# Kernel optimization log

Hardware: AMD Instinct MI355X
Metric: run time of the kernel (lower is better)

The kernel has to match this reference:

```python
import jax, jax.numpy as jnp
import numpy as np

NUM_MEMORIES = 4096
FEATURES = 4096
NUM_HEADS = 16
THRESHOLD = 1.0 / NUM_MEMORIES
EPSILON = 1e-12
COS_EPS = 1e-8
ENTROPY_COEF = 0.0002


def setup_inputs() -> dict:
    key = jax.random.key(0)
    ks = jax.random.split(key, 10)
    B, C, H, W = 256, 256, 4, 4
    F = FEATURES
    bound = float(np.sqrt(6.0 / F))  # kaiming_uniform fan_in = features
    x = jax.random.normal(ks[0], (B, C, H, W), dtype=jnp.float32)
    memory = jax.random.uniform(ks[1], (NUM_MEMORIES, F), minval=-bound, maxval=bound, dtype=jnp.float32)
    s = 0.02
    Wq = jax.random.normal(ks[2], (F, F), dtype=jnp.float32) * s
    Wk = jax.random.normal(ks[3], (F, F), dtype=jnp.float32) * s
    Wv = jax.random.normal(ks[4], (F, F), dtype=jnp.float32) * s
    Wo = jax.random.normal(ks[5], (F, F), dtype=jnp.float32) * s
    bq = jax.random.normal(ks[6], (F,), dtype=jnp.float32) * s
    bk = jax.random.normal(ks[7], (F,), dtype=jnp.float32) * s
    bv = jax.random.normal(ks[8], (F,), dtype=jnp.float32) * s
    bo = jax.random.normal(ks[9], (F,), dtype=jnp.float32) * s
    return {"x": x, "memory": memory, "Wq": Wq, "bq": bq, "Wk": Wk, "bk": bk,
            "Wv": Wv, "bv": bv, "Wo": Wo, "bo": bo}


def _mha(z, Wq, bq, Wk, bk, Wv, bv, Wo, bo):
    # z: [B, C, F] with C == 1 (seq_len = 1 here)
    B, C, F = z.shape
    dk = F // NUM_HEADS
    q = (z @ Wq + bq).reshape(B, C, NUM_HEADS, dk).transpose(0, 2, 1, 3)
    k = (z @ Wk + bk).reshape(B, C, NUM_HEADS, dk).transpose(0, 2, 1, 3)
    v = (z @ Wv + bv).reshape(B, C, NUM_HEADS, dk).transpose(0, 2, 1, 3)
    scores = jnp.einsum('bhqd,bhkd->bhqk', q, k) / jnp.sqrt(jnp.float32(dk))
    w = jax.nn.softmax(scores, axis=-1)
    o = jnp.einsum('bhqk,bhkd->bhqd', w, v).transpose(0, 2, 1, 3).reshape(B, C, F)
    return o @ Wo + bo


def reference(x, memory, Wq, bq, Wk, bk, Wv, bv, Wo, bo):
    B = x.shape[0]
    z = x.reshape(B, -1)[:, None, :]                      # [B, 1, F]
    z = _mha(z, Wq, bq, Wk, bk, Wv, bv, Wo, bo)[:, 0, :]  # [B, F]
    # cosine similarity against memory rows (torch eps = 1e-8, clamped per-vector)
    zn = jnp.maximum(jnp.linalg.norm(z, axis=1), COS_EPS)        # [B]
    mn = jnp.maximum(jnp.linalg.norm(memory, axis=1), COS_EPS)   # [M]
    mem_logit = (z @ memory.T) / (zn[:, None] * mn[None, :])     # [B, M]
    mem_weight = jax.nn.softmax(mem_logit, axis=1)
    # sparse shrinkage: relu(w - t) * w / (|w - t| + eps), then L1 renorm
    d = mem_weight - THRESHOLD
    mem_weight = jax.nn.relu(d) * mem_weight / (jnp.abs(d) + EPSILON)
    mem_weight = mem_weight / jnp.maximum(jnp.sum(jnp.abs(mem_weight), axis=1, keepdims=True), EPSILON)
    z_hat = (mem_weight @ memory).reshape(x.shape)
    entropy = -mem_weight * jnp.log(mem_weight + EPSILON)
    mem_loss = (entropy.sum() / B) * ENTROPY_COEF
    return (z_hat, mem_loss)
```

## Files before the change

### kernel.cpp

```cpp
#include <hip/hip_runtime.h>
#include <math.h>

#define MB 256
#define FF 4096

typedef __attribute__((ext_vector_type(8))) short short8v;
typedef __attribute__((ext_vector_type(4))) short short4v;
typedef __attribute__((ext_vector_type(16))) float f32x16;

__device__ __forceinline__ unsigned short bf16_rne(float f) {
    unsigned u = __builtin_bit_cast(unsigned, f);
    u += 0x7fffu + ((u >> 16) & 1u);
    return (unsigned short)(u >> 16);
}
__device__ __forceinline__ float bf16_f(unsigned short h) {
    unsigned u = ((unsigned)h) << 16;
    return __builtin_bit_cast(float, u);
}
__device__ __forceinline__ size_t apack_idx(int m, int k) {
    return ((size_t)(m >> 5) << 17) + ((size_t)(k >> 3) << 8)
         + ((m & 31) << 3) + (k & 7);
}

__device__ __forceinline__ float block_reduce_sum(float v, float* red) {
    const int tid = threadIdx.x;
    red[tid] = v; __syncthreads();
    for (int s = 128; s > 0; s >>= 1) {
        if (tid < s) red[tid] += red[tid + s];
        __syncthreads();
    }
    float r = red[0]; __syncthreads();
    return r;
}
__device__ __forceinline__ float block_reduce_max(float v, float* red) {
    const int tid = threadIdx.x;
    red[tid] = v; __syncthreads();
    for (int s = 128; s > 0; s >>= 1) {
        if (tid < s) red[tid] = fmaxf(red[tid], red[tid + s]);
        __syncthreads();
    }
    float r = red[0]; __syncthreads();
    return r;
}

__global__ __launch_bounds__(256) void rownorm_kernel(
    const float* __restrict__ src, float* __restrict__ dst, int ncols)
{
    __shared__ float red[256];
    const int row = blockIdx.x, tid = threadIdx.x;
    const float4* p = (const float4*)(src + (size_t)row * ncols);
    float s = 0.f;
    for (int i = tid; i < ncols / 4; i += 256) {
        float4 v = p[i];
        s += v.x * v.x + v.y * v.y + v.z * v.z + v.w * v.w;
    }
    float tot = block_reduce_sum(s, red);
    if (tid == 0) dst[row] = fmaxf(sqrtf(tot), 1e-8f);
}

__global__ __launch_bounds__(256) void split_plain(
    const float* __restrict__ src, unsigned short* __restrict__ hi,
    unsigned short* __restrict__ lo)
{
    const size_t i4 = (size_t)blockIdx.x * 256 + threadIdx.x;
    const size_t base = i4 * 4;
    const int m = (int)(base >> 12), k = (int)(base & 4095);
    const float4 v = *(const float4*)(src + base);
    unsigned short h0 = bf16_rne(v.x), h1 = bf16_rne(v.y), h2 = bf16_rne(v.z), h3 = bf16_rne(v.w);
    const size_t po = apack_idx(m, k);
    short4v hv = { (short)h0, (short)h1, (short)h2, (short)h3 };
    *(short4v*)(hi + po) = hv;
    short4v lv = { (short)bf16_rne(v.x - bf16_f(h0)), (short)bf16_rne(v.y - bf16_f(h1)),
                   (short)bf16_rne(v.z - bf16_f(h2)), (short)bf16_rne(v.w - bf16_f(h3)) };
    *(short4v*)(lo + po) = lv;
}

template <int BSRC, int SPLIT>
__global__ __launch_bounds__(512, 2) void gemm_sk(
    const unsigned short* __restrict__ Ah, const unsigned short* __restrict__ Al,
    const float* __restrict__ B, float* __restrict__ part)
{
    constexpr int PLANES = SPLIT ? 2 : 1;
    constexpr int BUFBYTES = PLANES * 8192;
    __shared__ char Bs[2 * BUFBYTES];

    const int tid = threadIdx.x;
    const int lane = tid & 63, w = tid >> 6;
    const int wm = w >> 1, wn = w & 1;
    const int bn0 = blockIdx.x * 128;
    const int k0 = blockIdx.z * 512;
    const int l31 = lane & 31;

    const float* bsrc;
    int gslot;
    if constexpr (BSRC == 0) {
        const int tk8 = tid >> 7, tn = tid & 127;
        bsrc = B + (size_t)(k0 + tk8 * 8) * FF + bn0 + tn;
        gslot = tid;
    } else {
        const int tn = tid >> 2, tk8 = tid & 3;
        bsrc = B + (size_t)(bn0 + tn) * FF + k0 + tk8 * 8;
        gslot = tk8 * 128 + tn;
    }

    float rB0, rB1, rB2, rB3, rB4, rB5, rB6, rB7;
    float sB0, sB1, sB2, sB3, sB4, sB5, sB6, sB7;

#define LOADB(S, T_)                                                          \
    {                                                                         \
        if constexpr (BSRC == 0) {                                            \
            const float* p_ = bsrc + (size_t)(T_) * 32 * FF;                  \
            S##B0 = p_[0 * FF]; S##B1 = p_[1 * FF];                           \
            S##B2 = p_[2 * FF]; S##B3 = p_[3 * FF];                           \
            S##B4 = p_[4 * FF]; S##B5 = p_[5 * FF];                           \
            S##B6 = p_[6 * FF]; S##B7 = p_[7 * FF];                           \
        } else {                                                              \
            const float* p_ = bsrc + (T_) * 32;                               \
            const float4 f0_ = *(const float4*)p_;                            \
            const float4 f1_ = *(const float4*)(p_ + 4);                      \
            S##B0 = f0_.x; S##B1 = f0_.y; S##B2 = f0_.z; S##B3 = f0_.w;       \
            S##B4 = f1_.x; S##B5 = f1_.y; S##B6 = f1_.z; S##B7 = f1_.w;       \
        }                                                                     \
    }

#define WRITEB(S, BUF_)                                                       \
    {                                                                         \
        unsigned short h0_ = bf16_rne(S##B0), h1_ = bf16_rne(S##B1),          \
                       h2_ = bf16_rne(S##B2), h3_ = bf16_rne(S##B3),          \
                       h4_ = bf16_rne(S##B4), h5_ = bf16_rne(S##B5),          \
                       h6_ = bf16_rne(S##B6), h7_ = bf16_rne(S##B7);          \
        short8v hv_ = { (short)h0_, (short)h1_, (short)h2_, (short)h3_,       \
                        (short)h4_, (short)h5_, (short)h6_, (short)h7_ };     \
        *(short8v*)(Bs + (BUF_) * BUFBYTES + gslot * 16) = hv_;               \
        if constexpr (SPLIT) {                                                \
            short8v lv_ = { (short)bf16_rne(S##B0 - bf16_f(h0_)),             \
                            (short)bf16_rne(S##B1 - bf16_f(h1_)),             \
                            (short)bf16_rne(S##B2 - bf16_f(h2_)),             \
                            (short)bf16_rne(S##B3 - bf16_f(h3_)),             \
                            (short)bf16_rne(S##B4 - bf16_f(h4_)),             \
                            (short)bf16_rne(S##B5 - bf16_f(h5_)),             \
                            (short)bf16_rne(S##B6 - bf16_f(h6_)),             \
                            (short)bf16_rne(S##B7 - bf16_f(h7_)) };           \
            *(short8v*)(Bs + (BUF_) * BUFBYTES + 8192 + gslot * 16) = lv_;    \
        }                                                                     \
    }

    const char* const fragbase =
        (const char*)Bs + (((lane >> 5) * 128) + wn * 64 + l31) * 16;
#define BFRAG(BUF_, P_, KH_, NS_)                                             \
    (*(const short8v*)(fragbase + (BUF_) * BUFBYTES + (P_) * 8192 + (KH_) * 4096 + (NS_) * 512))

    const size_t abase = ((size_t)(wm * 2) << 17) + ((size_t)blockIdx.z << 14)
                       + ((lane >> 5) << 8) + (l31 << 3);
    const unsigned short* pAh = Ah + abase;
    const unsigned short* pAl = SPLIT ? (Al + abase) : pAh;

    short8v cA_0h0, cA_0h1, cA_1h0, cA_1h1, cA_0l0, cA_0l1, cA_1l0, cA_1l1;
    short8v nA_0h0, nA_0h1, nA_1h0, nA_1h1, nA_0l0, nA_0l1, nA_1l0, nA_1l1;

#define LOADA(SET, T_)                                                        \
    {                                                                         \
        const int o_ = (T_) * 1024;                                           \
        SET##_0h0 = *(const short8v*)(pAh + o_);                              \
        SET##_0h1 = *(const short8v*)(pAh + o_ + 512);                        \
        SET##_1h0 = *(const short8v*)(pAh + 131072 + o_);                     \
        SET##_1h1 = *(const short8v*)(pAh + 131072 + o_ + 512);               \
        if constexpr (SPLIT) {                                                \
            SET##_0l0 = *(const short8v*)(pAl + o_);                          \
            SET##_0l1 = *(const short8v*)(pAl + o_ + 512);                    \
            SET##_1l0 = *(const short8v*)(pAl + 131072 + o_);                 \
            SET##_1l1 = *(const short8v*)(pAl + 131072 + o_ + 512);           \
        }                                                                     \
    }

    f32x16 acc00 = 0.0f, acc01 = 0.0f, acc10 = 0.0f, acc11 = 0.0f;

#define MFMA(A_, B_, C_) C_ = __builtin_amdgcn_mfma_f32_32x32x16_bf16(A_, B_, C_, 0, 0, 0)
#define MMKS(SET, BUF_, KH_)                                                  \
    {                                                                         \
        short8v bh0 = BFRAG(BUF_, 0, KH_, 0);                                 \
        short8v bh1 = BFRAG(BUF_, 0, KH_, 1);                                 \
        MFMA(SET##_0h##KH_, bh0, acc00); MFMA(SET##_0h##KH_, bh1, acc01);     \
        MFMA(SET##_1h##KH_, bh0, acc10); MFMA(SET##_1h##KH_, bh1, acc11);     \
        if constexpr (SPLIT) {                                                \
            short8v bl0 = BFRAG(BUF_, 1, KH_, 0);                             \
            short8v bl1 = BFRAG(BUF_, 1, KH_, 1);                             \
            MFMA(SET##_0h##KH_, bl0, acc00); MFMA(SET##_0h##KH_, bl1, acc01); \
            MFMA(SET##_1h##KH_, bl0, acc10); MFMA(SET##_1h##KH_, bl1, acc11); \
            MFMA(SET##_0l##KH_, bh0, acc00); MFMA(SET##_0l##KH_, bh1, acc01); \
            MFMA(SET##_1l##KH_, bh0, acc10); MFMA(SET##_1l##KH_, bh1, acc11); \
        }                                                                     \
    }

    LOADB(r, 0)
    LOADA(cA, 0)
    WRITEB(r, 0)
    __syncthreads();

#pragma unroll
    for (int tp = 0; tp < 8; ++tp) {
        const int t = tp * 2;
        LOADB(s, t + 1)
        LOADA(nA, t + 1)
        __builtin_amdgcn_s_setprio(1);
        MMKS(cA, 0, 0)
        MMKS(cA, 0, 1)
        __builtin_amdgcn_s_setprio(0);
        WRITEB(s, 1)
        __syncthreads();
        if (tp < 7) { LOADB(r, t + 2) LOADA(cA, t + 2) }
        __builtin_amdgcn_s_setprio(1);
        MMKS(nA, 1, 0)
        MMKS(nA, 1, 1)
        __builtin_amdgcn_s_setprio(0);
        if (tp < 7) { WRITEB(r, 0) }
        __syncthreads();
    }
#undef LOADB
#undef WRITEB
#undef BFRAG
#undef LOADA
#undef MFMA
#undef MMKS

    float* pp = part + (size_t)blockIdx.z * (MB * FF);
    const int rbase = wm * 64 + 4 * (lane >> 5);
    const int c0 = bn0 + wn * 64 + l31;
#pragma unroll
    for (int r = 0; r < 16; ++r) {
        const int row0 = rbase + (r & 3) + 8 * (r >> 2);
        float* rp0 = pp + (size_t)row0 * FF + c0;
        rp0[0]  = acc00[r];
        rp0[32] = acc01[r];
        float* rp1 = rp0 + (size_t)32 * FF;
        rp1[0]  = acc10[r];
        rp1[32] = acc11[r];
    }
}

template <int MODE>
__global__ __launch_bounds__(256) void reduce_k(
    const float* __restrict__ part, const float* __restrict__ bias,
    unsigned short* __restrict__ hi, unsigned short* __restrict__ lo,
    float* __restrict__ fout)
{
    const size_t idx4 = (size_t)blockIdx.x * 256 + threadIdx.x;
    const size_t base = idx4 * 4;
    float s0 = 0.f, s1 = 0.f, s2 = 0.f, s3 = 0.f;
#pragma unroll
    for (int c = 0; c < 8; ++c) {
        const float4 p = *(const float4*)(part + (size_t)c * (MB * FF) + base);
        s0 += p.x; s1 += p.y; s2 += p.z; s3 += p.w;
    }
    const int col = (int)(base & 4095);
    const int row = (int)(base >> 12);
    if constexpr (MODE == 0 || MODE == 1) {
        s0 += bias[col]; s1 += bias[col + 1]; s2 += bias[col + 2]; s3 += bias[col + 3];
        unsigned short h0 = bf16_rne(s0), h1 = bf16_rne(s1), h2 = bf16_rne(s2), h3 = bf16_rne(s3);
        const size_t po = apack_idx(row, col);
        short4v hv = { (short)h0, (short)h1, (short)h2, (short)h3 };
        *(short4v*)(hi + po) = hv;
        short4v lv = { (short)bf16_rne(s0 - bf16_f(h0)), (short)bf16_rne(s1 - bf16_f(h1)),
                       (short)bf16_rne(s2 - bf16_f(h2)), (short)bf16_rne(s3 - bf16_f(h3)) };
        *(short4v*)(lo + po) = lv;
        if constexpr (MODE == 1) {
            float4 o = { s0, s1, s2, s3 };
            *(float4*)(fout + base) = o;
        }
    } else {
        float4 o = { s0, s1, s2, s3 };
        *(float4*)(fout + base) = o;
    }
}

__global__ __launch_bounds__(256) void reduce_softmax(
    const float* __restrict__ part, const float* __restrict__ zn,
    const float* __restrict__ mn, unsigned short* __restrict__ w_hi,
    float* __restrict__ rowent)
{
    constexpr float THRESH = 1.0f / 4096.0f;
    constexpr float EPS = 1e-12f;
    __shared__ float srow[4096];
    __shared__ float red[256];
    const int row = blockIdx.x, tid = threadIdx.x;
    const float zr = zn[row];

    for (int i = tid; i < 1024; i += 256) {
        float s0 = 0.f, s1 = 0.f, s2 = 0.f, s3 = 0.f;
#pragma unroll
        for (int c = 0; c < 8; ++c) {
            const float4 p = *(const float4*)(part + (size_t)c * (MB * FF)
                                              + (size_t)row * FF + i * 4);
            s0 += p.x; s1 += p.y; s2 += p.z; s3 += p.w;
        }
        const float4 mv = *(const float4*)(mn + i * 4);
        float4 o = { s0 / (zr * mv.x), s1 / (zr * mv.y),
                     s2 / (zr * mv.z), s3 / (zr * mv.w) };
        *(float4*)(srow + i * 4) = o;
    }
    __syncthreads();

    float m = -INFINITY;
    for (int i = tid; i < FF; i += 256) m = fmaxf(m, srow[i]);
    m = block_reduce_max(m, red);

    float s = 0.f;
    for (int i = tid; i < FF; i += 256) {
        float e = expf(srow[i] - m);
        srow[i] = e; s += e;
    }
    s = block_reduce_sum(s, red);
    const float inv = 1.0f / s;

    float s2 = 0.f;
    for (int i = tid; i < FF; i += 256) {
        float ww = srow[i] * inv;
        float d = ww - THRESH;
        float w2 = fmaxf(d, 0.f) * ww / (fabsf(d) + EPS);
        srow[i] = w2; s2 += w2;
    }
    __syncthreads();
    s2 = block_reduce_sum(s2, red);
    const float inv2 = 1.0f / fmaxf(s2, EPS);

    float ent = 0.f;
    for (int i0 = tid * 8; i0 < FF; i0 += 2048) {
        unsigned short h[8];
#pragma unroll
        for (int j = 0; j < 8; ++j) {
            float w3 = srow[i0 + j] * inv2;
            h[j] = bf16_rne(w3);
            ent -= w3 * logf(w3 + EPS);
        }
        short8v hv = { (short)h[0], (short)h[1], (short)h[2], (short)h[3],
                       (short)h[4], (short)h[5], (short)h[6], (short)h[7] };
        *(short8v*)(w_hi + apack_idx(row, i0)) = hv;
    }
    ent = block_reduce_sum(ent, red);
    if (tid == 0) rowent[row] = ent;
}

__global__ __launch_bounds__(256) void loss_kernel(
    const float* __restrict__ rowent, float* __restrict__ out)
{
    __shared__ float red[256];
    const int tid = threadIdx.x;
    float tot = block_reduce_sum(rowent[tid], red);
    if (tid == 0) out[0] = (tot / 256.0f) * 0.0002f;
}

extern "C" void kernel_launch(void* const* d_in, const int* in_sizes, int n_in,
                              void* d_out, int out_size, void* d_ws, size_t ws_size,
                              hipStream_t stream)
{
    const float* x   = (const float*)d_in[0];
    const float* mem = (const float*)d_in[1];
    const float* Wv  = (const float*)d_in[6];
    const float* bv  = (const float*)d_in[7];
    const float* Wo  = (const float*)d_in[8];
    const float* bo  = (const float*)d_in[9];
    float* out = (float*)d_out;

    char* ws = (char*)d_ws;
    float*          part  = (float*)(ws + 134217728ull);
    unsigned short* x_hi  = (unsigned short*)(ws + 167772160ull);
    unsigned short* x_lo  = (unsigned short*)(ws + 169869312ull);
    unsigned short* v_hi  = (unsigned short*)(ws + 171966464ull);
    unsigned short* v_lo  = (unsigned short*)(ws + 174063616ull);
    unsigned short* o_hi  = (unsigned short*)(ws + 176160768ull);
    unsigned short* o_lo  = (unsigned short*)(ws + 178257920ull);
    float*          o_f32 = (float*)(ws + 180355072ull);
    unsigned short* w_hi  = (unsigned short*)(ws + 188743680ull);
    float*          zn    = (float*)(ws + 190840832ull);
    float*          mn    = zn + MB;
    float*          rowe  = mn + FF;

    const dim3 blk(256);
    const dim3 blkG(512);
    const dim3 gG(32, 1, 8);
    const int gR = (MB * FF) / (4 * 256);

    split_plain<<<gR, blk, 0, stream>>>(x, x_hi, x_lo);
    rownorm_kernel<<<FF, blk, 0, stream>>>(mem, mn, FF);

    gemm_sk<0, 1><<<gG, blkG, 0, stream>>>(x_hi, x_lo, Wv, part);
    reduce_k<0><<<gR, blk, 0, stream>>>(part, bv, v_hi, v_lo, nullptr);

    gemm_sk<0, 1><<<gG, blkG, 0, stream>>>(v_hi, v_lo, Wo, part);
    reduce_k<1><<<gR, blk, 0, stream>>>(part, bo, o_hi, o_lo, o_f32);

    rownorm_kernel<<<MB, blk, 0, stream>>>(o_f32, zn, FF);
    gemm_sk<1, 1><<<gG, blkG, 0, stream>>>(o_hi, o_lo, mem, part);
    reduce_softmax<<<MB, blk, 0, stream>>>(part, zn, mn, w_hi, rowe);

    gemm_sk<0, 0><<<gG, blkG, 0, stream>>>(w_hi, nullptr, mem, part);
    reduce_k<3><<<gR, blk, 0, stream>>>(part, nullptr, nullptr, nullptr, out);

    loss_kernel<<<1, blk, 0, stream>>>(rowe, out + (size_t)MB * FF);
}
```

Baseline: 180.6 us.

## Split GEMM M dimension across two blocks to halve per-warp tile and raise occupancy

Each GEMM block now covers 128 rows instead of all 256: a blockIdx.y of 2 selects the half, and each warp keeps one 32-row A tile instead of two. This halves the accumulator and A-fragment registers, so launch bounds now allow 4 blocks per CU, and the grid doubles to 512 blocks. In exchange, each B tile (including its on-the-fly bf16 hi/lo split) is loaded and converted twice, once per M half, adding global traffic and conversion work.

```diff
diff --git a/kernel.cpp b/kernel.cpp
--- a/kernel.cpp
+++ b/kernel.cpp
@@ -76,7 +76,7 @@
 }
 
 template <int BSRC, int SPLIT>
-__global__ __launch_bounds__(512, 2) void gemm_sk(
+__global__ __launch_bounds__(512, 4) void gemm_sk(
     const unsigned short* __restrict__ Ah, const unsigned short* __restrict__ Al,
     const float* __restrict__ B, float* __restrict__ part)
 {
@@ -150,45 +150,39 @@
 #define BFRAG(BUF_, P_, KH_, NS_)                                             \
     (*(const short8v*)(fragbase + (BUF_) * BUFBYTES + (P_) * 8192 + (KH_) * 4096 + (NS_) * 512))
 
-    const size_t abase = ((size_t)(wm * 2) << 17) + ((size_t)blockIdx.z << 14)
+    const size_t abase = ((size_t)(blockIdx.y * 4 + wm) << 17)
+                       + ((size_t)blockIdx.z << 14)
                        + ((lane >> 5) << 8) + (l31 << 3);
     const unsigned short* pAh = Ah + abase;
     const unsigned short* pAl = SPLIT ? (Al + abase) : pAh;
 
-    short8v cA_0h0, cA_0h1, cA_1h0, cA_1h1, cA_0l0, cA_0l1, cA_1l0, cA_1l1;
-    short8v nA_0h0, nA_0h1, nA_1h0, nA_1h1, nA_0l0, nA_0l1, nA_1l0, nA_1l1;
+    short8v cA_h0, cA_h1, cA_l0, cA_l1;
+    short8v nA_h0, nA_h1, nA_l0, nA_l1;
 
 #define LOADA(SET, T_)                                                        \
     {                                                                         \
         const int o_ = (T_) * 1024;                                           \
-        SET##_0h0 = *(const short8v*)(pAh + o_);                              \
-        SET##_0h1 = *(const short8v*)(pAh + o_ + 512);                        \
-        SET##_1h0 = *(const short8v*)(pAh + 131072 + o_);                     \
-        SET##_1h1 = *(const short8v*)(pAh + 131072 + o_ + 512);               \
+        SET##_h0 = *(const short8v*)(pAh + o_);                               \
+        SET##_h1 = *(const short8v*)(pAh + o_ + 512);                         \
         if constexpr (SPLIT) {                                                \
-            SET##_0l0 = *(const short8v*)(pAl + o_);                          \
-            SET##_0l1 = *(const short8v*)(pAl + o_ + 512);                    \
-            SET##_1l0 = *(const short8v*)(pAl + 131072 + o_);                 \
-            SET##_1l1 = *(const short8v*)(pAl + 131072 + o_ + 512);           \
+            SET##_l0 = *(const short8v*)(pAl + o_);                           \
+            SET##_l1 = *(const short8v*)(pAl + o_ + 512);                     \
         }                                                                     \
     }
 
-    f32x16 acc00 = 0.0f, acc01 = 0.0f, acc10 = 0.0f, acc11 = 0.0f;
+    f32x16 acc0 = 0.0f, acc1 = 0.0f;
 
 #define MFMA(A_, B_, C_) C_ = __builtin_amdgcn_mfma_f32_32x32x16_bf16(A_, B_, C_, 0, 0, 0)
 #define MMKS(SET, BUF_, KH_)                                                  \
     {                                                                         \
         short8v bh0 = BFRAG(BUF_, 0, KH_, 0);                                 \
         short8v bh1 = BFRAG(BUF_, 0, KH_, 1);                                 \
-        MFMA(SET##_0h##KH_, bh0, acc00); MFMA(SET##_0h##KH_, bh1, acc01);     \
-        MFMA(SET##_1h##KH_, bh0, acc10); MFMA(SET##_1h##KH_, bh1, acc11);     \
+        MFMA(SET##_h##KH_, bh0, acc0); MFMA(SET##_h##KH_, bh1, acc1);         \
         if constexpr (SPLIT) {                                                \
             short8v bl0 = BFRAG(BUF_, 1, KH_, 0);                             \
             short8v bl1 = BFRAG(BUF_, 1, KH_, 1);                             \
-            MFMA(SET##_0h##KH_, bl0, acc00); MFMA(SET##_0h##KH_, bl1, acc01); \
-            MFMA(SET##_1h##KH_, bl0, acc10); MFMA(SET##_1h##KH_, bl1, acc11); \
-            MFMA(SET##_0l##KH_, bh0, acc00); MFMA(SET##_0l##KH_, bh1, acc01); \
-            MFMA(SET##_1l##KH_, bh0, acc10); MFMA(SET##_1l##KH_, bh1, acc11); \
+            MFMA(SET##_h##KH_, bl0, acc0); MFMA(SET##_h##KH_, bl1, acc1);     \
+            MFMA(SET##_l##KH_, bh0, acc0); MFMA(SET##_l##KH_, bh1, acc1);     \
         }                                                                     \
     }
 
@@ -224,17 +218,14 @@
 #undef MMKS
 
     float* pp = part + (size_t)blockIdx.z * (MB * FF);
-    const int rbase = wm * 64 + 4 * (lane >> 5);
+    const int rbase = blockIdx.y * 128 + wm * 32 + 4 * (lane >> 5);
     const int c0 = bn0 + wn * 64 + l31;
 #pragma unroll
     for (int r = 0; r < 16; ++r) {
         const int row0 = rbase + (r & 3) + 8 * (r >> 2);
         float* rp0 = pp + (size_t)row0 * FF + c0;
-        rp0[0]  = acc00[r];
-        rp0[32] = acc01[r];
-        float* rp1 = rp0 + (size_t)32 * FF;
-        rp1[0]  = acc10[r];
-        rp1[32] = acc11[r];
+        rp0[0]  = acc0[r];
+        rp0[32] = acc1[r];
     }
 }
 
@@ -377,7 +368,7 @@
 
     const dim3 blk(256);
     const dim3 blkG(512);
-    const dim3 gG(32, 1, 8);
+    const dim3 gG(32, 2, 8);
     const int gR = (MB * FF) / (4 * 256);
 
     split_plain<<<gR, blk, 0, stream>>>(x, x_hi, x_lo);
```

Result: no change. 183.3 us (+1.5%).

## Stage two K-tiles per LDS buffer to halve barriers in split-K GEMM

Applied to the files above, without the earlier changes.

Doubles the shared-memory buffer so each stage holds two K-tiles, loads and writes B for both tiles together, and removes one __syncthreads per loop iteration. The goal is fewer barriers and longer prefetch distance for global B loads. In exchange the kernel uses twice the LDS and more live registers, which may reduce occupancy under the 512x2 launch bounds.

```diff
diff --git a/kernel.cpp b/kernel.cpp
--- a/kernel.cpp
+++ b/kernel.cpp
@@ -81,7 +81,8 @@
     const float* __restrict__ B, float* __restrict__ part)
 {
     constexpr int PLANES = SPLIT ? 2 : 1;
-    constexpr int BUFBYTES = PLANES * 8192;
+    constexpr int TILEBYTES = PLANES * 8192;
+    constexpr int BUFBYTES = 2 * TILEBYTES;
     __shared__ char Bs[2 * BUFBYTES];
 
     const int tid = threadIdx.x;
@@ -123,7 +124,7 @@
         }                                                                     \
     }
 
-#define WRITEB(S, BUF_)                                                       \
+#define WRITEB(S, BUF_, TS_)                                                  \
     {                                                                         \
         unsigned short h0_ = bf16_rne(S##B0), h1_ = bf16_rne(S##B1),          \
                        h2_ = bf16_rne(S##B2), h3_ = bf16_rne(S##B3),          \
@@ -131,7 +132,8 @@
                        h6_ = bf16_rne(S##B6), h7_ = bf16_rne(S##B7);          \
         short8v hv_ = { (short)h0_, (short)h1_, (short)h2_, (short)h3_,       \
                         (short)h4_, (short)h5_, (short)h6_, (short)h7_ };     \
-        *(short8v*)(Bs + (BUF_) * BUFBYTES + gslot * 16) = hv_;               \
+        char* d_ = Bs + (BUF_) * BUFBYTES + (TS_) * TILEBYTES + gslot * 16;   \
+        *(short8v*)d_ = hv_;                                                  \
         if constexpr (SPLIT) {                                                \
             short8v lv_ = { (short)bf16_rne(S##B0 - bf16_f(h0_)),             \
                             (short)bf16_rne(S##B1 - bf16_f(h1_)),             \
@@ -141,14 +143,15 @@
                             (short)bf16_rne(S##B5 - bf16_f(h5_)),             \
                             (short)bf16_rne(S##B6 - bf16_f(h6_)),             \
                             (short)bf16_rne(S##B7 - bf16_f(h7_)) };           \
-            *(short8v*)(Bs + (BUF_) * BUFBYTES + 8192 + gslot * 16) = lv_;    \
+            *(short8v*)(d_ + 8192) = lv_;                                     \
         }                                                                     \
     }
 
     const char* const fragbase =
         (const char*)Bs + (((lane >> 5) * 128) + wn * 64 + l31) * 16;
-#define BFRAG(BUF_, P_, KH_, NS_)                                             \
-    (*(const short8v*)(fragbase + (BUF_) * BUFBYTES + (P_) * 8192 + (KH_) * 4096 + (NS_) * 512))
+#define BFRAG(BUF_, TS_, P_, KH_, NS_)                                        \
+    (*(const short8v*)(fragbase + (BUF_) * BUFBYTES + (TS_) * TILEBYTES +     \
+                       (P_) * 8192 + (KH_) * 4096 + (NS_) * 512))
 
     const size_t abase = ((size_t)(wm * 2) << 17) + ((size_t)blockIdx.z << 14)
                        + ((lane >> 5) << 8) + (l31 << 3);
@@ -176,15 +179,15 @@
     f32x16 acc00 = 0.0f, acc01 = 0.0f, acc10 = 0.0f, acc11 = 0.0f;
 
 #define MFMA(A_, B_, C_) C_ = __builtin_amdgcn_mfma_f32_32x32x16_bf16(A_, B_, C_, 0, 0, 0)
-#define MMKS(SET, BUF_, KH_)                                                  \
+#define MMKS(SET, BUF_, TS_, KH_)                                             \
     {                                                                         \
-        short8v bh0 = BFRAG(BUF_, 0, KH_, 0);                                 \
-        short8v bh1 = BFRAG(BUF_, 0, KH_, 1);                                 \
+        short8v bh0 = BFRAG(BUF_, TS_, 0, KH_, 0);                            \
+        short8v bh1 = BFRAG(BUF_, TS_, 0, KH_, 1);                            \
         MFMA(SET##_0h##KH_, bh0, acc00); MFMA(SET##_0h##KH_, bh1, acc01);     \
         MFMA(SET##_1h##KH_, bh0, acc10); MFMA(SET##_1h##KH_, bh1, acc11);     \
         if constexpr (SPLIT) {                                                \
-            short8v bl0 = BFRAG(BUF_, 1, KH_, 0);                             \
-            short8v bl1 = BFRAG(BUF_, 1, KH_, 1);                             \
+            short8v bl0 = BFRAG(BUF_, TS_, 1, KH_, 0);                        \
+            short8v bl1 = BFRAG(BUF_, TS_, 1, KH_, 1);                        \
             MFMA(SET##_0h##KH_, bl0, acc00); MFMA(SET##_0h##KH_, bl1, acc01); \
             MFMA(SET##_1h##KH_, bl0, acc10); MFMA(SET##_1h##KH_, bl1, acc11); \
             MFMA(SET##_0l##KH_, bh0, acc00); MFMA(SET##_0l##KH_, bh1, acc01); \
@@ -193,27 +196,32 @@
     }
 
     LOADB(r, 0)
+    LOADB(s, 1)
     LOADA(cA, 0)
-    WRITEB(r, 0)
+    LOADA(nA, 1)
+    WRITEB(r, 0, 0)
+    WRITEB(s, 0, 1)
     __syncthreads();
 
 #pragma unroll
     for (int tp = 0; tp < 8; ++tp) {
+        const int cur = tp & 1, nxt = cur ^ 1;
         const int t = tp * 2;
-        LOADB(s, t + 1)
-        LOADA(nA, t + 1)
+        if (tp < 7) { LOADB(r, t + 2) LOADB(s, t + 3) }
         __builtin_amdgcn_s_setprio(1);
-        MMKS(cA, 0, 0)
-        MMKS(cA, 0, 1)
+        MMKS(cA, cur, 0, 0)
+        MMKS(cA, cur, 0, 1)
         __builtin_amdgcn_s_setprio(0);
-        WRITEB(s, 1)
-        __syncthreads();
-        if (tp < 7) { LOADB(r, t + 2) LOADA(cA, t + 2) }
+        if (tp < 7) { LOADA(cA, t + 2) }
         __builtin_amdgcn_s_setprio(1);
-        MMKS(nA, 1, 0)
-        MMKS(nA, 1, 1)
+        MMKS(nA, cur, 1, 0)
+        MMKS(nA, cur, 1, 1)
         __builtin_amdgcn_s_setprio(0);
-        if (tp < 7) { WRITEB(r, 0) }
+        if (tp < 7) {
+            LOADA(nA, t + 3)
+            WRITEB(r, nxt, 0)
+            WRITEB(s, nxt, 1)
+        }
         __syncthreads();
     }
 #undef LOADB
```

Result: slower. 188.1 us (+4.2%).
